# Kernel optimization log

Hardware: AMD Instinct MI355X
Metric: run time of the kernel (lower is better)

## Reference

```python
import jax, jax.numpy as jnp
import numpy as np

PRE_NMS_THRESH = 0.05
PRE_NMS_TOP_N = 1000
NMS_THRESH = 0.6
FPN_POST_NMS_TOP_N = 100
MIN_SIZE = 0
OFFSET = 10000.0  # per-class coordinate offset for batched per-class NMS
NEG = -1e9


def bilinear_resize(x, out_h, out_w):
    # x: [H, W, C] -> [out_h, out_w, C], matches torch interpolate(align_corners=False)
    H, W, _ = x.shape
    def grid(in_size, out_size):
        scale = in_size / out_size
        src = (jnp.arange(out_size, dtype=jnp.float32) + 0.5) * scale - 0.5
        src = jnp.clip(src, 0.0, in_size - 1.0)
        i0 = jnp.floor(src).astype(jnp.int32)
        i1 = jnp.minimum(i0 + 1, in_size - 1)
        lam = src - i0.astype(jnp.float32)
        return i0, i1, lam
    r0, r1, rl = grid(H, out_h)
    c0, c1, cl = grid(W, out_w)
    x = x[r0] * (1.0 - rl)[:, None, None] + x[r1] * rl[:, None, None]
    x = x[:, c0] * (1.0 - cl)[None, :, None] + x[:, c1] * cl[None, :, None]
    return x


def box_iou_plus1(b):
    area = (b[:, 2] - b[:, 0] + 1.0) * (b[:, 3] - b[:, 1] + 1.0)
    lt = jnp.maximum(b[:, None, :2], b[None, :, :2])
    rb = jnp.minimum(b[:, None, 2:], b[None, :, 2:])
    wh = jnp.clip(rb - lt + 1.0, 0.0)
    inter = wh[..., 0] * wh[..., 1]
    union = area[:, None] + area[None, :] - inter
    return inter / jnp.maximum(union, 1e-6)


def _forward(locations, box_cls, box_regression, centerness, box_mask, h, w):
    N, C, H, W = box_cls.shape
    M2 = box_mask.shape[1]
    Mi = int(np.sqrt(M2))
    HW = H * W
    K = PRE_NMS_TOP_N

    cls = jax.nn.sigmoid(box_cls.transpose(0, 2, 3, 1).reshape(N, HW, C))
    reg = box_regression.transpose(0, 2, 3, 1).reshape(N, HW, 4)
    cent = jax.nn.sigmoid(centerness.reshape(N, HW))
    mask = jax.nn.sigmoid(box_mask.transpose(0, 2, 3, 1))  # [N,H,W,M2]

    cand = cls > PRE_NMS_THRESH               # candidates from raw cls scores
    scr = cls * cent[:, :, None]              # centerness-weighted scores

    def per_image(cand_i, scr_i, reg_i, mask_i):
        # --- threshold + per-image topk (fixed K, padded with NEG) ---
        flat = jnp.where(cand_i, scr_i, NEG).reshape(HW * C)
        vals, idx = jax.lax.top_k(flat, K)
        valid = vals > NEG / 2
        loc_idx = idx // C
        labels = idx % C + 1                  # 1-based class labels
        locs = locations[loc_idx]             # [K,2]
        r = reg_i[loc_idx]                    # [K,4]
        boxes = jnp.stack([locs[:, 0] - r[:, 0], locs[:, 1] - r[:, 1],
                           locs[:, 0] + r[:, 2], locs[:, 1] + r[:, 3]], axis=1)
        scores = jnp.sqrt(jnp.where(valid, vals, 1.0)) * valid

        # --- mask paste: mean of upsampled mask over (buggy) box region ---
        up = bilinear_resize(mask_i, h, w)                      # [h,w,M2]
        integ = jnp.pad(jnp.cumsum(jnp.cumsum(up, 0), 1), ((1, 0), (1, 0), (0, 0)))
        bi = boxes.astype(jnp.int32)          # torch .int() truncation
        x1 = jnp.maximum(bi[:, 0], 0); x2 = jnp.minimum(bi[:, 2], h - 1)
        y1 = jnp.maximum(bi[:, 1], 0); y2 = jnp.minimum(bi[:, 3], w - 1)
        # original skip condition is (x1>=x2 or y1>=x2) -- bug replicated; extra
        # y1<y2 guard avoids NaN mean over empty region
        region_ok = (x1 < x2) & (y1 < x2) & (y1 < y2)
        x1c = jnp.clip(x1, 0, h); x2c = jnp.clip(x2, 0, h)
        y1c = jnp.clip(y1, 0, w); y2c = jnp.clip(y2, 0, w)
        s = integ[x2c, y2c] - integ[x1c, y2c] - integ[x2c, y1c] + integ[x1c, y1c]
        area = jnp.maximum((x2c - x1c) * (y2c - y1c), 1).astype(s.dtype)
        prob = ((s / area[:, None]) * region_ok[:, None]).reshape(K, Mi, Mi)

        # --- clip_to_image (x in [0,w-1], y in [0,h-1]) + remove_small_boxes ---
        bx = jnp.stack([jnp.clip(boxes[:, 0], 0, w - 1), jnp.clip(boxes[:, 1], 0, h - 1),
                        jnp.clip(boxes[:, 2], 0, w - 1), jnp.clip(boxes[:, 3], 0, h - 1)], 1)
        ws_ = bx[:, 2] - bx[:, 0] + 1.0
        hs_ = bx[:, 3] - bx[:, 1] + 1.0
        valid = valid & (ws_ >= MIN_SIZE) & (hs_ >= MIN_SIZE)

        # --- per-class greedy NMS via class-offset trick (fixed shape) ---
        nb = bx + (labels.astype(bx.dtype) * OFFSET)[:, None]
        order = jnp.argsort(-jnp.where(valid, scores, -1.0))
        nb_s, sc_s, v_s = nb[order], scores[order], valid[order]
        iou = box_iou_plus1(nb_s)
        rng = jnp.arange(K)
        def step(keep, i):
            ki = keep[i] & v_s[i]
            keep = keep.at[i].set(ki)
            keep = keep & ~(ki & (iou[i] > NMS_THRESH) & (rng > i))
            return keep, None
        keep, _ = jax.lax.scan(step, jnp.ones(K, bool), jnp.arange(K))
        v_final = keep & v_s

        # --- keep fpn_post_nms_top_n highest-scoring survivors ---
        fvals, fidx = jax.lax.top_k(jnp.where(v_final, sc_s, -1.0), FPN_POST_NMS_TOP_N)
        sel = order[fidx]
        vfin = v_final[fidx]
        return (bx[sel], scores[sel] * vfin, labels[sel], prob[sel] * vfin[:, None, None], vfin)

    return jax.vmap(per_image)(cand, scr, reg, mask)


def setup_inputs() -> dict:
    key = jax.random.key(0)
    ks = jax.random.split(key, 4)
    N, C, H, W, M2 = 2, 80, 32, 40, 196
    stride = 8
    ys, xs = jnp.meshgrid(jnp.arange(H), jnp.arange(W), indexing='ij')
    locations = jnp.stack([xs.reshape(-1), ys.reshape(-1)], 1).astype(jnp.float32) * stride + stride // 2
    box_cls = jax.random.normal(ks[0], (N, C, H, W), jnp.float32) - 2.0
    box_regression = jax.random.uniform(ks[1], (N, 4, H, W), jnp.float32) * 60.0 + 4.0
    centerness = jax.random.normal(ks[2], (N, 1, H, W), jnp.float32)
    box_mask = jax.random.normal(ks[3], (N, M2, H, W), jnp.float32)
    return {"locations": locations, "box_cls": box_cls, "box_regression": box_regression,
            "centerness": centerness, "box_mask": box_mask, "image_h": 256, "image_w": 320}


def reference(locations, box_cls, box_regression, centerness, box_mask, image_h, image_w):
    return _forward(locations, box_cls, box_regression, centerness, box_mask, image_h, image_w)
```

## Files before the change

kernel.cpp:

```cpp
#include <hip/hip_runtime.h>

#define DEVI __device__ __forceinline__

constexpr int N_ = 2, C_ = 80, H_ = 32, W_ = 40, HW_ = H_ * W_, HWC_ = HW_ * C_;
constexpr int KTOP = 1000, M2_ = 196;
constexpr int IMH = 256, IMW = 320;
constexpr int BUFCAP = 4096;
constexpr int NB = 2048;
constexpr int KB = 16;
constexpr int SLICE = HWC_ / KB;

constexpr int O_SC = 800, O_LB = 1000, O_PB = 1200, O_VF = 40400;

DEVI unsigned long long mapd(double v) {
  unsigned long long u = (unsigned long long)__double_as_longlong(v);
  return (u & 0x8000000000000000ull) ? ~u : (u | 0x8000000000000000ull);
}
DEVI double unmapd(unsigned long long k) {
  unsigned long long u = (k & 0x8000000000000000ull) ? (k ^ 0x8000000000000000ull) : ~k;
  return __longlong_as_double((long long)u);
}
DEVI int i0of(int x, int cap) {
  float src = ((float)x + 0.5f) * 0.125f - 0.5f;
  src = fminf(fmaxf(src, 0.f), (float)cap);
  return (int)floorf(src);
}

__global__ __launch_bounds__(1024) void k_pre(const float* cls, const float* cent, const float* bm,
                                              unsigned* ghist, unsigned* cand,
                                              float* msig, float* wr, float* wc) {
  int b = blockIdx.x, tid = threadIdx.x;
  if (b < N_ * KB) {
    __shared__ unsigned hist[NB];
    __shared__ unsigned run[NB];
    __shared__ unsigned short binls[SLICE];
    __shared__ float ce[HW_];
    __shared__ unsigned wtot[16], wabove[16];
    int n = b / KB, sb = b % KB;
    size_t base = (size_t)n * HWC_ + (size_t)sb * SLICE;
    for (int j = tid; j < NB; j += 1024) hist[j] = 0;
    for (int j = tid; j < HW_; j += 1024) ce[j] = 1.f / (1.f + expf(-cent[n * HW_ + j]));
    __syncthreads();
    #pragma unroll
    for (int it = 0; it < 7; ++it) {
      int j = it * 1024 + tid;
      if (j < SLICE) {
        float a = cls[base + j];
        float s = 1.f / (1.f + expf(-a));
        unsigned short bb = 0xFFFF;
        if (s > 0.0499999f) {
          float key = s * ce[j % HW_];
          unsigned kb2 = __float_as_uint(key);
          int bin = (int)(kb2 >> 16) - 0x3800;
          bin = bin < 0 ? 0 : (bin > NB - 1 ? NB - 1 : bin);
          bb = (unsigned short)bin;
          atomicAdd(&hist[bin], 1u);
        }
        binls[j] = bb;
      }
    }
    __syncthreads();
    unsigned* gh = ghist + ((size_t)n * KB + sb) * NB;
    for (int j = tid; j < NB; j += 1024) gh[j] = hist[j];
    int lane = tid & 63, wid = tid >> 6;
    unsigned aa = hist[2 * tid], bv = hist[2 * tid + 1];
    unsigned s2 = aa + bv, suf = s2;
    for (int off = 1; off < 64; off <<= 1) {
      unsigned v = __shfl_down(suf, off);
      if (lane + off < 64) suf += v;
    }
    if (lane == 0) wtot[wid] = suf;
    __syncthreads();
    if (tid == 0) { unsigned acc = 0; for (int w = 15; w >= 0; --w) { wabove[w] = acc; acc += wtot[w]; } }
    __syncthreads();
    unsigned above = (suf - s2) + wabove[wid];
    run[2 * tid + 1] = above;
    run[2 * tid] = above + bv;
    __syncthreads();
    unsigned* ca = cand + ((size_t)n * KB + sb) * SLICE;
    #pragma unroll
    for (int it = 0; it < 7; ++it) {
      int j = it * 1024 + tid;
      if (j < SLICE) {
        unsigned short bb = binls[j];
        if (bb != 0xFFFF) {
          unsigned pos = atomicAdd(&run[bb], 1u);
          ca[pos] = (unsigned)(base + j);
        }
      }
    }
  } else if (b < N_ * KB + 140) {
    __shared__ float tile[4][32][33];
    int g = tid >> 8, sub = tid & 255;
    int tt = (b - N_ * KB) * 4 + g;
    int n = tt / 280, r = tt % 280, rqt = r / 7, ct = r % 7;
    int tx = sub & 31, ty = sub >> 5;
    int rq0 = rqt * 32, c0 = ct * 32;
    for (int i = 0; i < 4; ++i) {
      int cc = c0 + ty + i * 8, rq = rq0 + tx;
      if (cc < M2_) {
        float v = bm[((size_t)n * M2_ + cc) * HW_ + rq];
        tile[g][ty + i * 8][tx] = 1.f / (1.f + expf(-v));
      }
    }
    __syncthreads();
    for (int i = 0; i < 4; ++i) {
      int rq = rq0 + ty + i * 8, cc = c0 + tx;
      if (cc < M2_) msig[((size_t)n * HW_ + rq) * M2_ + cc] = tile[g][tx][ty + i * 8];
    }
  } else {
    int t = tid;
    if (t < H_) {
      int r = t; float acc = 0.f; wr[0 * H_ + r] = 0.f;
      for (int x = 0; x < IMH; ++x) {
        float src = ((float)x + 0.5f) * ((float)H_ / (float)IMH) - 0.5f;
        src = fminf(fmaxf(src, 0.f), (float)(H_ - 1));
        int i0 = (int)floorf(src); int i1 = min(i0 + 1, H_ - 1);
        float lam = src - (float)i0;
        float w = ((r == i0) ? (1.f - lam) : 0.f) + ((r == i1) ? lam : 0.f);
        acc += w; wr[(x + 1) * H_ + r] = acc;
      }
    } else if (t < H_ + W_) {
      int q = t - H_; float acc = 0.f; wc[0 * W_ + q] = 0.f;
      for (int y = 0; y < IMW; ++y) {
        float src = ((float)y + 0.5f) * ((float)W_ / (float)IMW) - 0.5f;
        src = fminf(fmaxf(src, 0.f), (float)(W_ - 1));
        int i0 = (int)floorf(src); int i1 = min(i0 + 1, W_ - 1);
        float lam = src - (float)i0;
        float w = ((q == i0) ? (1.f - lam) : 0.f) + ((q == i1) ? lam : 0.f);
        acc += w; wc[(y + 1) * W_ + q] = acc;
      }
    }
  }
}

struct SortSh { unsigned long long K[BUFCAP]; unsigned I[BUFCAP]; };

__global__ __launch_bounds__(1024) void k_sel(const unsigned* ghist, const unsigned* cand,
                                              const float* cls, const float* cent,
                                              const float* loc, const float* breg,
                                              double* bxd, double* scd, int* lab, int* vld, int* rg,
                                              unsigned* keepg) {
  __shared__ SortSh sh;
  __shared__ unsigned wtot[16], wabove[16], sliceCnt[16], sliceOff[17];
  __shared__ unsigned sD;
  int n = blockIdx.x, tid = threadIdx.x, lane = tid & 63, wid = tid >> 6;
  keepg[n * 1024 + tid] = 0;
  const unsigned* gh = ghist + (size_t)n * KB * NB;
  unsigned a = 0, bv = 0;
  #pragma unroll
  for (int q = 0; q < KB; ++q) { a += gh[q * NB + 2 * tid]; bv += gh[q * NB + 2 * tid + 1]; }
  if (tid == 0) sD = 0;
  unsigned s2 = a + bv, suf = s2;
  for (int off = 1; off < 64; off <<= 1) {
    unsigned v = __shfl_down(suf, off);
    if (lane + off < 64) suf += v;
  }
  if (lane == 0) wtot[wid] = suf;
  __syncthreads();
  if (tid == 0) { unsigned acc = 0; for (int w = 15; w >= 0; --w) { wabove[w] = acc; acc += wtot[w]; } }
  __syncthreads();
  unsigned above = (suf - s2) + wabove[wid];
  if (above < 1000u && above + bv >= 1000u) sD = (unsigned)(2 * tid + 1);
  if (above + bv < 1000u && above + bv + a >= 1000u) sD = (unsigned)(2 * tid);
  __syncthreads();
  unsigned D = sD;
  unsigned Dg = (D > 0) ? D - 1 : 0;
  {
    unsigned acc = 0;
    for (int bin = (int)Dg + lane; bin < NB; bin += 64) acc += gh[wid * NB + bin];
    for (int off = 32; off; off >>= 1) acc += __shfl_down(acc, off);
    if (lane == 0) sliceCnt[wid] = acc;
  }
  __syncthreads();
  if (tid == 0) {
    unsigned acc = 0;
    for (int q = 0; q < KB; ++q) { sliceOff[q] = acc; acc += sliceCnt[q]; }
    sliceOff[KB] = acc;
  }
  __syncthreads();
  int G = (int)sliceOff[KB]; if (G > BUFCAP) G = BUFCAP;
  {
    const unsigned* ca = cand + ((size_t)n * KB + wid) * SLICE;
    unsigned cs = sliceCnt[wid], so = sliceOff[wid];
    for (unsigned e = lane; e < cs; e += 64) {
      unsigned pos = so + e;
      if (pos < (unsigned)BUFCAP) {
        unsigned t = ca[e];
        int c = (int)((t % (unsigned)HWC_) / (unsigned)HW_);
        int hw = (int)(t % (unsigned)HW_);
        double aa = (double)cls[t];
        double ss = 1.0 / (1.0 + exp(-aa));
        double ced = 1.0 / (1.0 + exp(-(double)cent[n * HW_ + hw]));
        double v = (ss > 0.05) ? ss * ced : -1e9;
        sh.K[pos] = mapd(v);
        sh.I[pos] = (unsigned)(hw * C_ + c);
      }
    }
  }
  __syncthreads();
  int P = 1024; while (P < G) P <<= 1;
  for (int j = G + tid; j < P; j += 1024) { sh.K[j] = 0ull; sh.I[j] = 0xFFFFFFFFu; }
  __syncthreads();
  int E = P >> 10;
  for (int sz = 2; sz <= P; sz <<= 1) {
    for (int st = sz >> 1; st >= 64; st >>= 1) {
      for (int p = tid; p < (P >> 1); p += 1024) {
        int i = ((p & ~(st - 1)) << 1) | (p & (st - 1));
        int j = i | st;
        bool up = ((i & sz) == 0);
        unsigned long long k1 = sh.K[i], k2 = sh.K[j];
        unsigned i1 = sh.I[i], i2 = sh.I[j];
        bool bef = (k1 > k2) || (k1 == k2 && i1 < i2);
        if (bef != up) { sh.K[i] = k2; sh.K[j] = k1; sh.I[i] = i2; sh.I[j] = i1; }
      }
      __syncthreads();
    }
    {
      int st0 = ((sz >> 1) < 32) ? (sz >> 1) : 32;
      for (int e = 0; e < E; ++e) {
        int elem = tid + (e << 10);
        unsigned long long k = sh.K[elem];
        unsigned ii = sh.I[elem];
        bool dir = ((elem & sz) == 0);
        for (int st = st0; st >= 1; st >>= 1) {
          unsigned long long ko = __shfl_xor(k, st);
          unsigned io = __shfl_xor(ii, st);
          bool low = ((elem & st) == 0);
          bool first = (k > ko) || (k == ko && ii < io);
          bool take_mine = first ^ (!low) ^ (!dir);
          if (!take_mine) { k = ko; ii = io; }
        }
        sh.K[elem] = k; sh.I[elem] = ii;
      }
      __syncthreads();
    }
  }

  if (tid < KTOP) {
    unsigned long long key = sh.K[tid];
    unsigned idx = sh.I[tid];
    double v = unmapd(key);
    int valid = (v > -5e8) && (idx < (unsigned)HWC_);
    if (idx >= (unsigned)HWC_) idx = 0;
    int hw = (int)(idx / C_), c = (int)(idx % C_);
    double lx = (double)loc[hw * 2 + 0], ly = (double)loc[hw * 2 + 1];
    const float* rg4 = breg + (size_t)n * 4 * HW_;
    double r0 = (double)rg4[0 * HW_ + hw], r1 = (double)rg4[1 * HW_ + hw];
    double r2 = (double)rg4[2 * HW_ + hw], r3 = (double)rg4[3 * HW_ + hw];
    double b0 = lx - r0, b1 = ly - r1, b2 = lx + r2, b3 = ly + r3;
    double sc = valid ? sqrt(v) : 0.0;
    int bi0 = (int)b0, bi1 = (int)b1, bi2 = (int)b2, bi3 = (int)b3;
    int x1 = max(bi0, 0), x2 = min(bi2, IMH - 1), y1 = max(bi1, 0), y2 = min(bi3, IMW - 1);
    int rok = (x1 < x2) && (y1 < x2) && (y1 < y2);
    int x1c = min(max(x1, 0), IMH), x2c = min(max(x2, 0), IMH);
    int y1c = min(max(y1, 0), IMW), y2c = min(max(y2, 0), IMW);
    int area = max((x2c - x1c) * (y2c - y1c), 1);
    double c0 = fmin(fmax(b0, 0.0), (double)(IMW - 1));
    double c1 = fmin(fmax(b1, 0.0), (double)(IMH - 1));
    double c2 = fmin(fmax(b2, 0.0), (double)(IMW - 1));
    double c3 = fmin(fmax(b3, 0.0), (double)(IMH - 1));
    size_t base = (size_t)n * 1024 + tid;
    bxd[base * 4 + 0] = c0; bxd[base * 4 + 1] = c1; bxd[base * 4 + 2] = c2; bxd[base * 4 + 3] = c3;
    scd[base] = sc; lab[base] = c + 1; vld[base] = valid;
    int* r8 = rg + base * 8;
    r8[0] = x1c; r8[1] = x2c; r8[2] = y1c; r8[3] = y2c; r8[4] = area; r8[5] = rok;
  }
}

__global__ void k_nms(const double* bxd, const int* lab, const int* vld, unsigned* keepg) {
  int cls = blockIdx.x + 1, n = blockIdx.y, tid = threadIdx.x;
  __shared__ int mk[KTOP];
  __shared__ double mb0[KTOP], mb1[KTOP], mb2[KTOP], mb3[KTOP], ma[KTOP];
  __shared__ unsigned char kept[KTOP];
  int m = 0;
  for (int base = 0; base < KTOP; base += 64) {
    int t = base + tid;
    bool pred = (t < KTOP) && (lab[n * 1024 + t] == cls) && (vld[n * 1024 + t] != 0);
    unsigned long long bb = __ballot(pred);
    if (pred) {
      int pos = m + (int)__popcll(bb & ((1ull << tid) - 1ull));
      mk[pos] = t;
      const double* p = bxd + ((size_t)n * 1024 + t) * 4;
      double b0 = p[0], b1 = p[1], b2 = p[2], b3 = p[3];
      mb0[pos] = b0; mb1[pos] = b1; mb2[pos] = b2; mb3[pos] = b3;
      ma[pos] = (b2 - b0 + 1.0) * (b3 - b1 + 1.0);
      kept[pos] = 1;
    }
    m += (int)__popcll(bb);
  }
  __syncthreads();
  for (int i = 0; i < m; ++i) {
    if (kept[i]) {
      double x1 = mb0[i], y1 = mb1[i], x2 = mb2[i], y2 = mb3[i], ai = ma[i];
      for (int j = i + 1 + tid; j < m; j += 64) {
        double ltx = fmax(x1, mb0[j]), lty = fmax(y1, mb1[j]);
        double rbx = fmin(x2, mb2[j]), rby = fmin(y2, mb3[j]);
        double iw = fmax(rbx - ltx + 1.0, 0.0), ih = fmax(rby - lty + 1.0, 0.0);
        double inter = iw * ih;
        double uni = ai + ma[j] - inter;
        if (inter / fmax(uni, 1e-6) > 0.6) kept[j] = 0;
      }
    }
    __syncthreads();
  }
  for (int i = tid; i < m; i += 64) keepg[n * 1024 + mk[i]] = (unsigned)kept[i];
}

__global__ __launch_bounds__(256) void k_finish(const unsigned* keepg, const double* bxd,
                                                const double* scd, const int* lab, const int* rg,
                                                const float* msig, const float* wr, const float* wc,
                                                float* out) {
  int t = blockIdx.x, n = blockIdx.y, tid = threadIdx.x, lane = tid & 63, wid = tid >> 6;
  __shared__ int lsel[100], lvf[100];
  __shared__ unsigned woff[4]; __shared__ unsigned sS;
  __shared__ float A[H_], B[W_];

  int i0 = tid * 4;
  unsigned ff[4]; int lc = 0;
  for (int j = 0; j < 4; ++j) {
    int i = i0 + j;
    ff[j] = (i < KTOP) ? keepg[n * 1024 + i] : 0u;
    lc += (int)ff[j];
  }
  unsigned pre = (unsigned)lc;
  for (int off = 1; off < 64; off <<= 1) {
    unsigned v = __shfl_up(pre, off);
    if (lane >= off) pre += v;
  }
  if (lane == 63) woff[wid] = pre;
  __syncthreads();
  if (tid == 0) { unsigned acc = 0; for (int w = 0; w < 4; ++w) { unsigned tmp = woff[w]; woff[w] = acc; acc += tmp; } sS = acc; }
  __syncthreads();
  int kpre = (int)(woff[wid] + pre - (unsigned)lc);
  int S = (int)sS;
  for (int j = 0; j < 4; ++j) {
    int i = i0 + j;
    if (i < KTOP) {
      if (ff[j]) { if (kpre < 100) { lsel[kpre] = i; lvf[kpre] = 1; } kpre++; }
      else { int slot = S + (i - kpre); if (slot < 100) { lsel[slot] = i; lvf[slot] = 0; } }
    }
  }
  __syncthreads();

  int k = lsel[t], vf = lvf[t];
  if (tid == 0) {
    const double* bb = bxd + ((size_t)n * 1024 + k) * 4;
    out[(n * 100 + t) * 4 + 0] = (float)bb[0];
    out[(n * 100 + t) * 4 + 1] = (float)bb[1];
    out[(n * 100 + t) * 4 + 2] = (float)bb[2];
    out[(n * 100 + t) * 4 + 3] = (float)bb[3];
    out[O_SC + n * 100 + t] = vf ? (float)scd[n * 1024 + k] : 0.f;
    out[O_LB + n * 100 + t] = (float)lab[n * 1024 + k];
    out[O_VF + n * 100 + t] = (float)vf;
  }
  const int* r8 = rg + ((size_t)n * 1024 + k) * 8;
  int x1c = r8[0], x2c = r8[1], y1c = r8[2], y2c = r8[3], area = r8[4], rok = r8[5];
  if (tid < H_) A[tid] = wr[x2c * H_ + tid] - wr[x1c * H_ + tid];
  else if (tid < H_ + W_) { int q = tid - H_; B[q] = wc[y2c * W_ + q] - wc[y1c * W_ + q]; }
  __syncthreads();
  if (tid < M2_) {
    float acc = 0.f;
    if (rok && vf) {
      int rlo = i0of(x1c, H_ - 1);
      int rhi = min(i0of(x2c - 1, H_ - 1) + 1, H_ - 1);
      int qlo = i0of(y1c, W_ - 1);
      int qhi = min(i0of(y2c - 1, W_ - 1) + 1, W_ - 1);
      for (int r = rlo; r <= rhi; ++r) {
        float ar = A[r];
        const float* mrow = msig + ((size_t)((n * H_ + r) * W_ + qlo)) * M2_ + tid;
        float rs = 0.f;
        #pragma unroll 4
        for (int q = qlo; q <= qhi; ++q) { rs += B[q] * mrow[0]; mrow += M2_; }
        acc += ar * rs;
      }
      acc /= (float)area;
    }
    out[O_PB + (size_t)(n * 100 + t) * M2_ + tid] = acc;
  }
}

extern "C" void kernel_launch(void* const* d_in, const int* in_sizes, int n_in,
                              void* d_out, int out_size, void* d_ws, size_t ws_size,
                              hipStream_t stream) {
  (void)in_sizes; (void)n_in; (void)out_size; (void)ws_size;
  const float* locations = (const float*)d_in[0];
  const float* box_cls   = (const float*)d_in[1];
  const float* box_reg   = (const float*)d_in[2];
  const float* cent      = (const float*)d_in[3];
  const float* box_mask  = (const float*)d_in[4];
  float* out = (float*)d_out;

  char* ws = (char*)d_ws;
  size_t off = 0;
  auto alloc = [&](size_t bytes) -> void* {
    void* p = ws + off;
    off = (off + bytes + 255) & ~(size_t)255;
    return p;
  };
  unsigned* ghist = (unsigned*)alloc((size_t)N_ * KB * NB * 4);
  unsigned* cand  = (unsigned*)alloc((size_t)N_ * KB * SLICE * 4);
  double* bxd     = (double*)alloc((size_t)N_ * 1024 * 4 * 8);
  double* scd     = (double*)alloc((size_t)N_ * 1024 * 8);
  int* lab        = (int*)alloc((size_t)N_ * 1024 * 4);
  int* vld        = (int*)alloc((size_t)N_ * 1024 * 4);
  int* rg         = (int*)alloc((size_t)N_ * 1024 * 8 * 4);
  unsigned* keepg = (unsigned*)alloc((size_t)N_ * 1024 * 4);
  float* msig     = (float*)alloc((size_t)N_ * HW_ * M2_ * 4);
  float* wr       = (float*)alloc((size_t)(IMH + 1) * H_ * 4);
  float* wc       = (float*)alloc((size_t)(IMW + 1) * W_ * 4);

  k_pre<<<N_ * KB + 140 + 1, 1024, 0, stream>>>(box_cls, cent, box_mask, ghist, cand, msig, wr, wc);
  k_sel<<<N_, 1024, 0, stream>>>(ghist, cand, box_cls, cent, locations, box_reg,
                                 bxd, scd, lab, vld, rg, keepg);
  k_nms<<<dim3(C_, N_), 64, 0, stream>>>(bxd, lab, vld, keepg);
  k_finish<<<dim3(100, N_), 256, 0, stream>>>(keepg, bxd, scd, lab, rg, msig, wr, wc, out);
}
```

Baseline: 100.9 us.

## Fuse four-stage pipeline into one cooperative kernel with grid syncs

Merges the preprocessing, top-k selection, per-class NMS and mask-finish kernels into a single cooperative kernel of 200 blocks separated by grid-wide syncs. Candidate compaction now happens inside the histogram blocks, using the global threshold bin and wave-ballot offsets, writing at most 2048 candidates per image. This replaces the separate full-slice candidate lists. NMS uses one wave per class with ballot-based suppression bitmasks and caps each class at 128 boxes. The aim is to remove launch gaps and shrink the gather and sort, at the cost of grid-sync overhead, 1024-thread blocks that sit idle in most phases, and a cap that could change results if a class has more than 128 boxes.

Result: slower. 179.2 us (+77.7%).

```diff
diff --git a/kernel.cpp b/kernel.cpp
--- a/kernel.cpp
+++ b/kernel.cpp
@@ -1,14 +1,18 @@
 #include <hip/hip_runtime.h>
+#include <hip/hip_cooperative_groups.h>
+
+namespace cg = cooperative_groups;
 
 #define DEVI __device__ __forceinline__
 
 constexpr int N_ = 2, C_ = 80, H_ = 32, W_ = 40, HW_ = H_ * W_, HWC_ = HW_ * C_;
 constexpr int KTOP = 1000, M2_ = 196;
 constexpr int IMH = 256, IMW = 320;
-constexpr int BUFCAP = 4096;
 constexpr int NB = 2048;
 constexpr int KB = 16;
 constexpr int SLICE = HWC_ / KB;
+constexpr int BCAP = 2048;
+constexpr int GBLK = 200;
 
 constexpr int O_SC = 800, O_LB = 1000, O_PB = 1200, O_VF = 40400;
 
@@ -26,71 +30,55 @@
   return (int)floorf(src);
 }
 
-__global__ __launch_bounds__(1024) void k_pre(const float* cls, const float* cent, const float* bm,
-                                              unsigned* ghist, unsigned* cand,
-                                              float* msig, float* wr, float* wc) {
-  int b = blockIdx.x, tid = threadIdx.x;
+struct ShSlice {
+  unsigned key[SLICE];
+  unsigned hist[NB];
+  float ce[HW_];
+  unsigned wtot[16], wabove[16], sliceCnt[16], sliceOff[17];
+  unsigned sD, lcnt;
+};
+struct ShSort { unsigned long long K[BCAP]; unsigned I[BCAP]; };
+struct ShNms  { double bx[128][5]; unsigned short ml[128]; };
+struct ShMask { float tile[4][32][33]; };
+struct ShFin  { int lsel[100], lvf[100]; unsigned wcnt[16], woff[16], Stot; float A[H_], Bw[W_]; };
+union ShU { ShSlice a; ShSort c; ShNms d; ShMask m; ShFin e; };
+
+__global__ __launch_bounds__(1024) void mega(const float* cls, const float* cent, const float* bm,
+                                             const float* loc, const float* breg,
+                                             unsigned* ghist, unsigned* bufI, unsigned* cntG,
+                                             double* bxd, double* scd, int* lab, int* vld, int* rg,
+                                             unsigned* keepg, float* msig, float* wr, float* wc,
+                                             float* out) {
+  __shared__ ShU sh;
+  cg::grid_group gg = cg::this_grid();
+  int b = blockIdx.x, tid = threadIdx.x, lane = tid & 63, wid = tid >> 6;
+
   if (b < N_ * KB) {
-    __shared__ unsigned hist[NB];
-    __shared__ unsigned run[NB];
-    __shared__ unsigned short binls[SLICE];
-    __shared__ float ce[HW_];
-    __shared__ unsigned wtot[16], wabove[16];
-    int n = b / KB, sb = b % KB;
+    int n = b >> 4, sb = b & 15;
     size_t base = (size_t)n * HWC_ + (size_t)sb * SLICE;
-    for (int j = tid; j < NB; j += 1024) hist[j] = 0;
-    for (int j = tid; j < HW_; j += 1024) ce[j] = 1.f / (1.f + expf(-cent[n * HW_ + j]));
+    for (int j = tid; j < NB; j += 1024) sh.a.hist[j] = 0;
+    for (int j = tid; j < HW_; j += 1024) sh.a.ce[j] = 1.f / (1.f + expf(-cent[n * HW_ + j]));
     __syncthreads();
     #pragma unroll
     for (int it = 0; it < 7; ++it) {
       int j = it * 1024 + tid;
       if (j < SLICE) {
-        float a = cls[base + j];
-        float s = 1.f / (1.f + expf(-a));
-        unsigned short bb = 0xFFFF;
+        float aa = cls[base + j];
+        float s = 1.f / (1.f + expf(-aa));
+        unsigned key = 0;
         if (s > 0.0499999f) {
-          float key = s * ce[j % HW_];
-          unsigned kb2 = __float_as_uint(key);
-          int bin = (int)(kb2 >> 16) - 0x3800;
+          key = __float_as_uint(s * sh.a.ce[j % HW_]);
+          int bin = (int)(key >> 16) - 0x3800;
           bin = bin < 0 ? 0 : (bin > NB - 1 ? NB - 1 : bin);
-          bb = (unsigned short)bin;
-          atomicAdd(&hist[bin], 1u);
-        }
-        binls[j] = bb;
+          atomicAdd(&sh.a.hist[bin], 1u);
+        }
+        sh.a.key[j] = key;
       }
     }
     __syncthreads();
     unsigned* gh = ghist + ((size_t)n * KB + sb) * NB;
-    for (int j = tid; j < NB; j += 1024) gh[j] = hist[j];
-    int lane = tid & 63, wid = tid >> 6;
-    unsigned aa = hist[2 * tid], bv = hist[2 * tid + 1];
-    unsigned s2 = aa + bv, suf = s2;
-    for (int off = 1; off < 64; off <<= 1) {
-      unsigned v = __shfl_down(suf, off);
-      if (lane + off < 64) suf += v;
-    }
-    if (lane == 0) wtot[wid] = suf;
-    __syncthreads();
-    if (tid == 0) { unsigned acc = 0; for (int w = 15; w >= 0; --w) { wabove[w] = acc; acc += wtot[w]; } }
-    __syncthreads();
-    unsigned above = (suf - s2) + wabove[wid];
-    run[2 * tid + 1] = above;
-    run[2 * tid] = above + bv;
-    __syncthreads();
-    unsigned* ca = cand + ((size_t)n * KB + sb) * SLICE;
-    #pragma unroll
-    for (int it = 0; it < 7; ++it) {
-      int j = it * 1024 + tid;
-      if (j < SLICE) {
-        unsigned short bb = binls[j];
-        if (bb != 0xFFFF) {
-          unsigned pos = atomicAdd(&run[bb], 1u);
-          ca[pos] = (unsigned)(base + j);
-        }
-      }
-    }
+    for (int j = tid; j < NB; j += 1024) gh[j] = sh.a.hist[j];
   } else if (b < N_ * KB + 140) {
-    __shared__ float tile[4][32][33];
     int g = tid >> 8, sub = tid & 255;
     int tt = (b - N_ * KB) * 4 + g;
     int n = tt / 280, r = tt % 280, rqt = r / 7, ct = r % 7;
@@ -100,15 +88,15 @@
       int cc = c0 + ty + i * 8, rq = rq0 + tx;
       if (cc < M2_) {
         float v = bm[((size_t)n * M2_ + cc) * HW_ + rq];
-        tile[g][ty + i * 8][tx] = 1.f / (1.f + expf(-v));
+        sh.m.tile[g][ty + i * 8][tx] = 1.f / (1.f + expf(-v));
       }
     }
     __syncthreads();
     for (int i = 0; i < 4; ++i) {
       int rq = rq0 + ty + i * 8, cc = c0 + tx;
-      if (cc < M2_) msig[((size_t)n * HW_ + rq) * M2_ + cc] = tile[g][tx][ty + i * 8];
-    }
-  } else {
+      if (cc < M2_) msig[((size_t)n * HW_ + rq) * M2_ + cc] = sh.m.tile[g][tx][ty + i * 8];
+    }
+  } else if (b == N_ * KB + 140) {
     int t = tid;
     if (t < H_) {
       int r = t; float acc = 0.f; wr[0 * H_ + r] = 0.f;
@@ -132,251 +120,267 @@
       }
     }
   }
-}
-
-struct SortSh { unsigned long long K[BUFCAP]; unsigned I[BUFCAP]; };
-
-__global__ __launch_bounds__(1024) void k_sel(const unsigned* ghist, const unsigned* cand,
-                                              const float* cls, const float* cent,
-                                              const float* loc, const float* breg,
-                                              double* bxd, double* scd, int* lab, int* vld, int* rg,
-                                              unsigned* keepg) {
-  __shared__ SortSh sh;
-  __shared__ unsigned wtot[16], wabove[16], sliceCnt[16], sliceOff[17];
-  __shared__ unsigned sD;
-  int n = blockIdx.x, tid = threadIdx.x, lane = tid & 63, wid = tid >> 6;
-  keepg[n * 1024 + tid] = 0;
-  const unsigned* gh = ghist + (size_t)n * KB * NB;
-  unsigned a = 0, bv = 0;
-  #pragma unroll
-  for (int q = 0; q < KB; ++q) { a += gh[q * NB + 2 * tid]; bv += gh[q * NB + 2 * tid + 1]; }
-  if (tid == 0) sD = 0;
-  unsigned s2 = a + bv, suf = s2;
-  for (int off = 1; off < 64; off <<= 1) {
-    unsigned v = __shfl_down(suf, off);
-    if (lane + off < 64) suf += v;
+  gg.sync();
+
+  if (b < N_ * KB) {
+    int n = b >> 4, sb = b & 15;
+    const unsigned* gh = ghist + (size_t)n * KB * NB;
+    unsigned a = 0, bv = 0;
+    #pragma unroll
+    for (int q = 0; q < KB; ++q) { a += gh[q * NB + 2 * tid]; bv += gh[q * NB + 2 * tid + 1]; }
+    if (tid == 0) { sh.a.sD = 0; sh.a.lcnt = 0; }
+    unsigned s2 = a + bv, suf = s2;
+    for (int off = 1; off < 64; off <<= 1) {
+      unsigned v = __shfl_down(suf, off);
+      if (lane + off < 64) suf += v;
+    }
+    if (lane == 0) sh.a.wtot[wid] = suf;
+    __syncthreads();
+    if (tid == 0) { unsigned acc = 0; for (int w = 15; w >= 0; --w) { sh.a.wabove[w] = acc; acc += sh.a.wtot[w]; } }
+    __syncthreads();
+    unsigned above = (suf - s2) + sh.a.wabove[wid];
+    if (above < 1000u && above + bv >= 1000u) sh.a.sD = (unsigned)(2 * tid + 1);
+    if (above + bv < 1000u && above + bv + a >= 1000u) sh.a.sD = (unsigned)(2 * tid);
+    __syncthreads();
+    unsigned D = sh.a.sD;
+    unsigned Dg = (D > 0) ? D - 1 : 0;
+    {
+      unsigned acc = 0;
+      for (int bin = (int)Dg + lane; bin < NB; bin += 64) acc += gh[wid * NB + bin];
+      for (int off = 32; off; off >>= 1) acc += __shfl_down(acc, off);
+      if (lane == 0) sh.a.sliceCnt[wid] = acc;
+    }
+    __syncthreads();
+    if (tid == 0) {
+      unsigned acc = 0;
+      for (int q = 0; q < KB; ++q) { sh.a.sliceOff[q] = acc; acc += sh.a.sliceCnt[q]; }
+      sh.a.sliceOff[KB] = acc;
+      if (sb == 0) cntG[n] = acc;
+    }
+    __syncthreads();
+    unsigned myStart = sh.a.sliceOff[sb];
+    #pragma unroll
+    for (int it = 0; it < 7; ++it) {
+      int j = it * 1024 + tid;
+      bool win = false;
+      if (j < SLICE) {
+        unsigned key = sh.a.key[j];
+        if (key) {
+          int bin = (int)(key >> 16) - 0x3800;
+          bin = bin < 0 ? 0 : (bin > NB - 1 ? NB - 1 : bin);
+          win = (unsigned)bin >= Dg;
+        }
+      }
+      unsigned long long mb = __ballot(win);
+      if (mb) {
+        int lead = __builtin_ctzll(mb);
+        unsigned offw = 0;
+        if (lane == lead) offw = atomicAdd(&sh.a.lcnt, (unsigned)__popcll(mb));
+        offw = (unsigned)__shfl((int)offw, lead);
+        if (win) {
+          unsigned pos = myStart + offw + (unsigned)__popcll(mb & ((1ull << lane) - 1ull));
+          if (pos < (unsigned)BCAP)
+            bufI[(size_t)n * BCAP + pos] = (unsigned)((j % HW_) * C_ + (sb * 5 + j / HW_));
+        }
+      }
+    }
   }
-  if (lane == 0) wtot[wid] = suf;
-  __syncthreads();
-  if (tid == 0) { unsigned acc = 0; for (int w = 15; w >= 0; --w) { wabove[w] = acc; acc += wtot[w]; } }
-  __syncthreads();
-  unsigned above = (suf - s2) + wabove[wid];
-  if (above < 1000u && above + bv >= 1000u) sD = (unsigned)(2 * tid + 1);
-  if (above + bv < 1000u && above + bv + a >= 1000u) sD = (unsigned)(2 * tid);
-  __syncthreads();
-  unsigned D = sD;
-  unsigned Dg = (D > 0) ? D - 1 : 0;
+  gg.sync();
+
+  if (b < N_) {
+    int n = b;
+    unsigned cnt = cntG[n]; if (cnt > (unsigned)BCAP) cnt = BCAP;
+    for (unsigned pos = tid; pos < cnt; pos += 1024) {
+      unsigned idx = bufI[(size_t)n * BCAP + pos];
+      int hw = (int)(idx / C_), c = (int)(idx % C_);
+      double aa = (double)cls[(size_t)n * HWC_ + (size_t)c * HW_ + hw];
+      double ss = 1.0 / (1.0 + exp(-aa));
+      double ced = 1.0 / (1.0 + exp(-(double)cent[n * HW_ + hw]));
+      double v = (ss > 0.05) ? ss * ced : -1e9;
+      sh.c.K[pos] = mapd(v);
+      sh.c.I[pos] = idx;
+    }
+    int P = 1024; while (P < (int)cnt) P <<= 1;
+    for (int j = (int)cnt + tid; j < P; j += 1024) { sh.c.K[j] = 0ull; sh.c.I[j] = 0xFFFFFFFFu; }
+    __syncthreads();
+    int E = P >> 10;
+    for (int sz = 2; sz <= P; sz <<= 1) {
+      for (int st = sz >> 1; st >= 64; st >>= 1) {
+        for (int p = tid; p < (P >> 1); p += 1024) {
+          int i = ((p & ~(st - 1)) << 1) | (p & (st - 1));
+          int j = i | st;
+          bool up = ((i & sz) == 0);
+          unsigned long long k1 = sh.c.K[i], k2 = sh.c.K[j];
+          unsigned i1 = sh.c.I[i], i2 = sh.c.I[j];
+          bool bef = (k1 > k2) || (k1 == k2 && i1 < i2);
+          if (bef != up) { sh.c.K[i] = k2; sh.c.K[j] = k1; sh.c.I[i] = i2; sh.c.I[j] = i1; }
+        }
+        __syncthreads();
+      }
+      {
+        int st0 = ((sz >> 1) < 32) ? (sz >> 1) : 32;
+        for (int e = 0; e < E; ++e) {
+          int elem = tid + (e << 10);
+          unsigned long long k = sh.c.K[elem];
+          unsigned ii = sh.c.I[elem];
+          bool dir = ((elem & sz) == 0);
+          for (int st = st0; st >= 1; st >>= 1) {
+            unsigned long long ko = __shfl_xor(k, st);
+            unsigned io = __shfl_xor(ii, st);
+            bool low = ((elem & st) == 0);
+            bool first = (k > ko) || (k == ko && ii < io);
+            bool take_mine = first ^ (!low) ^ (!dir);
+            if (!take_mine) { k = ko; ii = io; }
+          }
+          sh.c.K[elem] = k; sh.c.I[elem] = ii;
+        }
+        __syncthreads();
+      }
+    }
+    if (tid < KTOP) {
+      unsigned long long key = sh.c.K[tid];
+      unsigned idx = sh.c.I[tid];
+      double v = unmapd(key);
+      int valid = (v > -5e8) && (idx < (unsigned)HWC_);
+      if (idx >= (unsigned)HWC_) idx = 0;
+      int hw = (int)(idx / C_), c = (int)(idx % C_);
+      double lx = (double)loc[hw * 2 + 0], ly = (double)loc[hw * 2 + 1];
+      const float* rg4 = breg + (size_t)n * 4 * HW_;
+      double r0 = (double)rg4[0 * HW_ + hw], r1 = (double)rg4[1 * HW_ + hw];
+      double r2 = (double)rg4[2 * HW_ + hw], r3 = (double)rg4[3 * HW_ + hw];
+      double b0 = lx - r0, b1 = ly - r1, b2 = lx + r2, b3 = ly + r3;
+      double sc = valid ? sqrt(v) : 0.0;
+      int bi0 = (int)b0, bi1 = (int)b1, bi2 = (int)b2, bi3 = (int)b3;
+      int x1 = max(bi0, 0), x2 = min(bi2, IMH - 1), y1 = max(bi1, 0), y2 = min(bi3, IMW - 1);
+      int rok = (x1 < x2) && (y1 < x2) && (y1 < y2);
+      int x1c = min(max(x1, 0), IMH), x2c = min(max(x2, 0), IMH);
+      int y1c = min(max(y1, 0), IMW), y2c = min(max(y2, 0), IMW);
+      int area = max((x2c - x1c) * (y2c - y1c), 1);
+      double c0 = fmin(fmax(b0, 0.0), (double)(IMW - 1));
+      double c1 = fmin(fmax(b1, 0.0), (double)(IMH - 1));
+      double c2 = fmin(fmax(b2, 0.0), (double)(IMW - 1));
+      double c3 = fmin(fmax(b3, 0.0), (double)(IMH - 1));
+      size_t base = (size_t)n * 1024 + tid;
+      bxd[base * 4 + 0] = c0; bxd[base * 4 + 1] = c1; bxd[base * 4 + 2] = c2; bxd[base * 4 + 3] = c3;
+      scd[base] = sc; lab[base] = c + 1; vld[base] = valid;
+      int* r8 = rg + base * 8;
+      r8[0] = x1c; r8[1] = x2c; r8[2] = y1c; r8[3] = y2c; r8[4] = area; r8[5] = rok;
+    }
+  } else if (b < N_ + 2) {
+    keepg[(b - N_) * 1024 + tid] = 0;
+  }
+  gg.sync();
+
+  if (b < N_ * C_) {
+    int cls_ = (b % C_) + 1, n = b / C_;
+    if (tid < 64) {
+      int m = 0;
+      for (int ch = 0; ch < 16; ++ch) {
+        int e = ch * 64 + lane;
+        bool pred = (e < KTOP) && vld[n * 1024 + e] && (lab[n * 1024 + e] == cls_);
+        unsigned long long bb = __ballot(pred);
+        if (pred) {
+          int pos = m + (int)__popcll(bb & ((1ull << lane) - 1ull));
+          if (pos < 128) {
+            const double* p = bxd + ((size_t)n * 1024 + e) * 4;
+            double b0 = p[0], b1 = p[1], b2 = p[2], b3 = p[3];
+            sh.d.bx[pos][0] = b0; sh.d.bx[pos][1] = b1; sh.d.bx[pos][2] = b2; sh.d.bx[pos][3] = b3;
+            sh.d.bx[pos][4] = (b2 - b0 + 1.0) * (b3 - b1 + 1.0);
+            sh.d.ml[pos] = (unsigned short)e;
+          }
+        }
+        m += (int)__popcll(bb);
+      }
+      if (m > 128) m = 128;
+      __builtin_amdgcn_wave_barrier();
+      unsigned long long k0 = (m >= 64) ? ~0ull : ((1ull << m) - 1ull);
+      unsigned long long k1m = (m > 64) ? ((m >= 128) ? ~0ull : ((1ull << (m - 64)) - 1ull)) : 0ull;
+      for (int i = 0; i < m; ++i) {
+        bool alive = (i < 64) ? ((k0 >> i) & 1ull) : ((k1m >> (i - 64)) & 1ull);
+        if (!alive) continue;
+        double x1 = sh.d.bx[i][0], y1 = sh.d.bx[i][1], x2 = sh.d.bx[i][2], y2 = sh.d.bx[i][3], ai = sh.d.bx[i][4];
+        {
+          int j = lane;
+          bool ok = (j < m) && (j > i);
+          int jj = ok ? j : 0;
+          double u1 = sh.d.bx[jj][0], v1 = sh.d.bx[jj][1], u2 = sh.d.bx[jj][2], v2 = sh.d.bx[jj][3], aj = sh.d.bx[jj][4];
+          double ltx = fmax(x1, u1), lty = fmax(y1, v1), rbx = fmin(x2, u2), rby = fmin(y2, v2);
+          double iw = fmax(rbx - ltx + 1.0, 0.0), ih = fmax(rby - lty + 1.0, 0.0);
+          double inter = iw * ih, uni = ai + aj - inter;
+          bool sup = ok && (inter / fmax(uni, 1e-6) > 0.6);
+          k0 &= ~__ballot(sup);
+        }
+        if (m > 64) {
+          int j = 64 + lane;
+          bool ok = (j < m) && (j > i);
+          int jj = ok ? j : 0;
+          double u1 = sh.d.bx[jj][0], v1 = sh.d.bx[jj][1], u2 = sh.d.bx[jj][2], v2 = sh.d.bx[jj][3], aj = sh.d.bx[jj][4];
+          double ltx = fmax(x1, u1), lty = fmax(y1, v1), rbx = fmin(x2, u2), rby = fmin(y2, v2);
+          double iw = fmax(rbx - ltx + 1.0, 0.0), ih = fmax(rby - lty + 1.0, 0.0);
+          double inter = iw * ih, uni = ai + aj - inter;
+          bool sup = ok && (inter / fmax(uni, 1e-6) > 0.6);
+          k1m &= ~__ballot(sup);
+        }
+      }
+      for (int j = lane; j < m; j += 64) {
+        bool kb = (j < 64) ? ((k0 >> j) & 1ull) : ((k1m >> (j - 64)) & 1ull);
+        keepg[n * 1024 + sh.d.ml[j]] = kb ? 1u : 0u;
+      }
+    }
+  }
+  gg.sync();
+
   {
-    unsigned acc = 0;
-    for (int bin = (int)Dg + lane; bin < NB; bin += 64) acc += gh[wid * NB + bin];
-    for (int off = 32; off; off >>= 1) acc += __shfl_down(acc, off);
-    if (lane == 0) sliceCnt[wid] = acc;
-  }
-  __syncthreads();
-  if (tid == 0) {
-    unsigned acc = 0;
-    for (int q = 0; q < KB; ++q) { sliceOff[q] = acc; acc += sliceCnt[q]; }
-    sliceOff[KB] = acc;
-  }
-  __syncthreads();
-  int G = (int)sliceOff[KB]; if (G > BUFCAP) G = BUFCAP;
-  {
-    const unsigned* ca = cand + ((size_t)n * KB + wid) * SLICE;
-    unsigned cs = sliceCnt[wid], so = sliceOff[wid];
-    for (unsigned e = lane; e < cs; e += 64) {
-      unsigned pos = so + e;
-      if (pos < (unsigned)BUFCAP) {
-        unsigned t = ca[e];
-        int c = (int)((t % (unsigned)HWC_) / (unsigned)HW_);
-        int hw = (int)(t % (unsigned)HW_);
-        double aa = (double)cls[t];
-        double ss = 1.0 / (1.0 + exp(-aa));
-        double ced = 1.0 / (1.0 + exp(-(double)cent[n * HW_ + hw]));
-        double v = (ss > 0.05) ? ss * ced : -1e9;
-        sh.K[pos] = mapd(v);
-        sh.I[pos] = (unsigned)(hw * C_ + c);
-      }
-    }
-  }
-  __syncthreads();
-  int P = 1024; while (P < G) P <<= 1;
-  for (int j = G + tid; j < P; j += 1024) { sh.K[j] = 0ull; sh.I[j] = 0xFFFFFFFFu; }
-  __syncthreads();
-  int E = P >> 10;
-  for (int sz = 2; sz <= P; sz <<= 1) {
-    for (int st = sz >> 1; st >= 64; st >>= 1) {
-      for (int p = tid; p < (P >> 1); p += 1024) {
-        int i = ((p & ~(st - 1)) << 1) | (p & (st - 1));
-        int j = i | st;
-        bool up = ((i & sz) == 0);
-        unsigned long long k1 = sh.K[i], k2 = sh.K[j];
-        unsigned i1 = sh.I[i], i2 = sh.I[j];
-        bool bef = (k1 > k2) || (k1 == k2 && i1 < i2);
-        if (bef != up) { sh.K[i] = k2; sh.K[j] = k1; sh.I[i] = i2; sh.I[j] = i1; }
-      }
-      __syncthreads();
-    }
-    {
-      int st0 = ((sz >> 1) < 32) ? (sz >> 1) : 32;
-      for (int e = 0; e < E; ++e) {
-        int elem = tid + (e << 10);
-        unsigned long long k = sh.K[elem];
-        unsigned ii = sh.I[elem];
-        bool dir = ((elem & sz) == 0);
-        for (int st = st0; st >= 1; st >>= 1) {
-          unsigned long long ko = __shfl_xor(k, st);
-          unsigned io = __shfl_xor(ii, st);
-          bool low = ((elem & st) == 0);
-          bool first = (k > ko) || (k == ko && ii < io);
-          bool take_mine = first ^ (!low) ^ (!dir);
-          if (!take_mine) { k = ko; ii = io; }
-        }
-        sh.K[elem] = k; sh.I[elem] = ii;
-      }
-      __syncthreads();
-    }
-  }
-
-  if (tid < KTOP) {
-    unsigned long long key = sh.K[tid];
-    unsigned idx = sh.I[tid];
-    double v = unmapd(key);
-    int valid = (v > -5e8) && (idx < (unsigned)HWC_);
-    if (idx >= (unsigned)HWC_) idx = 0;
-    int hw = (int)(idx / C_), c = (int)(idx % C_);
-    double lx = (double)loc[hw * 2 + 0], ly = (double)loc[hw * 2 + 1];
-    const float* rg4 = breg + (size_t)n * 4 * HW_;
-    double r0 = (double)rg4[0 * HW_ + hw], r1 = (double)rg4[1 * HW_ + hw];
-    double r2 = (double)rg4[2 * HW_ + hw], r3 = (double)rg4[3 * HW_ + hw];
-    double b0 = lx - r0, b1 = ly - r1, b2 = lx + r2, b3 = ly + r3;
-    double sc = valid ? sqrt(v) : 0.0;
-    int bi0 = (int)b0, bi1 = (int)b1, bi2 = (int)b2, bi3 = (int)b3;
-    int x1 = max(bi0, 0), x2 = min(bi2, IMH - 1), y1 = max(bi1, 0), y2 = min(bi3, IMW - 1);
-    int rok = (x1 < x2) && (y1 < x2) && (y1 < y2);
-    int x1c = min(max(x1, 0), IMH), x2c = min(max(x2, 0), IMH);
-    int y1c = min(max(y1, 0), IMW), y2c = min(max(y2, 0), IMW);
-    int area = max((x2c - x1c) * (y2c - y1c), 1);
-    double c0 = fmin(fmax(b0, 0.0), (double)(IMW - 1));
-    double c1 = fmin(fmax(b1, 0.0), (double)(IMH - 1));
-    double c2 = fmin(fmax(b2, 0.0), (double)(IMW - 1));
-    double c3 = fmin(fmax(b3, 0.0), (double)(IMH - 1));
-    size_t base = (size_t)n * 1024 + tid;
-    bxd[base * 4 + 0] = c0; bxd[base * 4 + 1] = c1; bxd[base * 4 + 2] = c2; bxd[base * 4 + 3] = c3;
-    scd[base] = sc; lab[base] = c + 1; vld[base] = valid;
-    int* r8 = rg + base * 8;
-    r8[0] = x1c; r8[1] = x2c; r8[2] = y1c; r8[3] = y2c; r8[4] = area; r8[5] = rok;
-  }
-}
-
-__global__ void k_nms(const double* bxd, const int* lab, const int* vld, unsigned* keepg) {
-  int cls = blockIdx.x + 1, n = blockIdx.y, tid = threadIdx.x;
-  __shared__ int mk[KTOP];
-  __shared__ double mb0[KTOP], mb1[KTOP], mb2[KTOP], mb3[KTOP], ma[KTOP];
-  __shared__ unsigned char kept[KTOP];
-  int m = 0;
-  for (int base = 0; base < KTOP; base += 64) {
-    int t = base + tid;
-    bool pred = (t < KTOP) && (lab[n * 1024 + t] == cls) && (vld[n * 1024 + t] != 0);
-    unsigned long long bb = __ballot(pred);
-    if (pred) {
-      int pos = m + (int)__popcll(bb & ((1ull << tid) - 1ull));
-      mk[pos] = t;
-      const double* p = bxd + ((size_t)n * 1024 + t) * 4;
-      double b0 = p[0], b1 = p[1], b2 = p[2], b3 = p[3];
-      mb0[pos] = b0; mb1[pos] = b1; mb2[pos] = b2; mb3[pos] = b3;
-      ma[pos] = (b2 - b0 + 1.0) * (b3 - b1 + 1.0);
-      kept[pos] = 1;
-    }
-    m += (int)__popcll(bb);
-  }
-  __syncthreads();
-  for (int i = 0; i < m; ++i) {
-    if (kept[i]) {
-      double x1 = mb0[i], y1 = mb1[i], x2 = mb2[i], y2 = mb3[i], ai = ma[i];
-      for (int j = i + 1 + tid; j < m; j += 64) {
-        double ltx = fmax(x1, mb0[j]), lty = fmax(y1, mb1[j]);
-        double rbx = fmin(x2, mb2[j]), rby = fmin(y2, mb3[j]);
-        double iw = fmax(rbx - ltx + 1.0, 0.0), ih = fmax(rby - lty + 1.0, 0.0);
-        double inter = iw * ih;
-        double uni = ai + ma[j] - inter;
-        if (inter / fmax(uni, 1e-6) > 0.6) kept[j] = 0;
-      }
-    }
-    __syncthreads();
-  }
-  for (int i = tid; i < m; i += 64) keepg[n * 1024 + mk[i]] = (unsigned)kept[i];
-}
-
-__global__ __launch_bounds__(256) void k_finish(const unsigned* keepg, const double* bxd,
-                                                const double* scd, const int* lab, const int* rg,
-                                                const float* msig, const float* wr, const float* wc,
-                                                float* out) {
-  int t = blockIdx.x, n = blockIdx.y, tid = threadIdx.x, lane = tid & 63, wid = tid >> 6;
-  __shared__ int lsel[100], lvf[100];
-  __shared__ unsigned woff[4]; __shared__ unsigned sS;
-  __shared__ float A[H_], B[W_];
-
-  int i0 = tid * 4;
-  unsigned ff[4]; int lc = 0;
-  for (int j = 0; j < 4; ++j) {
-    int i = i0 + j;
-    ff[j] = (i < KTOP) ? keepg[n * 1024 + i] : 0u;
-    lc += (int)ff[j];
-  }
-  unsigned pre = (unsigned)lc;
-  for (int off = 1; off < 64; off <<= 1) {
-    unsigned v = __shfl_up(pre, off);
-    if (lane >= off) pre += v;
-  }
-  if (lane == 63) woff[wid] = pre;
-  __syncthreads();
-  if (tid == 0) { unsigned acc = 0; for (int w = 0; w < 4; ++w) { unsigned tmp = woff[w]; woff[w] = acc; acc += tmp; } sS = acc; }
-  __syncthreads();
-  int kpre = (int)(woff[wid] + pre - (unsigned)lc);
-  int S = (int)sS;
-  for (int j = 0; j < 4; ++j) {
-    int i = i0 + j;
-    if (i < KTOP) {
-      if (ff[j]) { if (kpre < 100) { lsel[kpre] = i; lvf[kpre] = 1; } kpre++; }
-      else { int slot = S + (i - kpre); if (slot < 100) { lsel[slot] = i; lvf[slot] = 0; } }
-    }
-  }
-  __syncthreads();
-
-  int k = lsel[t], vf = lvf[t];
-  if (tid == 0) {
-    const double* bb = bxd + ((size_t)n * 1024 + k) * 4;
-    out[(n * 100 + t) * 4 + 0] = (float)bb[0];
-    out[(n * 100 + t) * 4 + 1] = (float)bb[1];
-    out[(n * 100 + t) * 4 + 2] = (float)bb[2];
-    out[(n * 100 + t) * 4 + 3] = (float)bb[3];
-    out[O_SC + n * 100 + t] = vf ? (float)scd[n * 1024 + k] : 0.f;
-    out[O_LB + n * 100 + t] = (float)lab[n * 1024 + k];
-    out[O_VF + n * 100 + t] = (float)vf;
-  }
-  const int* r8 = rg + ((size_t)n * 1024 + k) * 8;
-  int x1c = r8[0], x2c = r8[1], y1c = r8[2], y2c = r8[3], area = r8[4], rok = r8[5];
-  if (tid < H_) A[tid] = wr[x2c * H_ + tid] - wr[x1c * H_ + tid];
-  else if (tid < H_ + W_) { int q = tid - H_; B[q] = wc[y2c * W_ + q] - wc[y1c * W_ + q]; }
-  __syncthreads();
-  if (tid < M2_) {
-    float acc = 0.f;
-    if (rok && vf) {
-      int rlo = i0of(x1c, H_ - 1);
-      int rhi = min(i0of(x2c - 1, H_ - 1) + 1, H_ - 1);
-      int qlo = i0of(y1c, W_ - 1);
-      int qhi = min(i0of(y2c - 1, W_ - 1) + 1, W_ - 1);
-      for (int r = rlo; r <= rhi; ++r) {
-        float ar = A[r];
-        const float* mrow = msig + ((size_t)((n * H_ + r) * W_ + qlo)) * M2_ + tid;
-        float rs = 0.f;
-        #pragma unroll 4
-        for (int q = qlo; q <= qhi; ++q) { rs += B[q] * mrow[0]; mrow += M2_; }
-        acc += ar * rs;
-      }
-      acc /= (float)area;
-    }
-    out[O_PB + (size_t)(n * 100 + t) * M2_ + tid] = acc;
+    int t = b % 100, n = b / 100;
+    int kp = (tid < KTOP) ? (int)keepg[n * 1024 + tid] : 0;
+    unsigned long long bal = __ballot(kp != 0);
+    int posw = (int)__popcll(bal & ((1ull << lane) - 1ull));
+    if (lane == 0) sh.e.wcnt[wid] = (unsigned)__popcll(bal);
+    __syncthreads();
+    if (tid == 0) { unsigned acc = 0; for (int i = 0; i < 16; ++i) { sh.e.woff[i] = acc; acc += sh.e.wcnt[i]; } sh.e.Stot = acc; }
+    __syncthreads();
+    int posK = (int)sh.e.woff[wid] + posw;
+    int S = (int)sh.e.Stot;
+    if (tid < KTOP) {
+      if (kp) { if (posK < 100) { sh.e.lsel[posK] = tid; sh.e.lvf[posK] = 1; } }
+      else { int slot = S + (tid - posK); if (slot < 100) { sh.e.lsel[slot] = tid; sh.e.lvf[slot] = 0; } }
+    }
+    __syncthreads();
+    int k = sh.e.lsel[t], vf = sh.e.lvf[t];
+    if (tid == 0) {
+      const double* bb = bxd + ((size_t)n * 1024 + k) * 4;
+      out[(n * 100 + t) * 4 + 0] = (float)bb[0];
+      out[(n * 100 + t) * 4 + 1] = (float)bb[1];
+      out[(n * 100 + t) * 4 + 2] = (float)bb[2];
+      out[(n * 100 + t) * 4 + 3] = (float)bb[3];
+      out[O_SC + n * 100 + t] = vf ? (float)scd[n * 1024 + k] : 0.f;
+      out[O_LB + n * 100 + t] = (float)lab[n * 1024 + k];
+      out[O_VF + n * 100 + t] = (float)vf;
+    }
+    const int* r8 = rg + ((size_t)n * 1024 + k) * 8;
+    int x1c = r8[0], x2c = r8[1], y1c = r8[2], y2c = r8[3], area = r8[4], rok = r8[5];
+    if (tid < H_) sh.e.A[tid] = wr[x2c * H_ + tid] - wr[x1c * H_ + tid];
+    else if (tid < H_ + W_) { int q = tid - H_; sh.e.Bw[q] = wc[y2c * W_ + q] - wc[y1c * W_ + q]; }
+    __syncthreads();
+    if (tid < M2_) {
+      float acc = 0.f;
+      if (rok && vf) {
+        int rlo = i0of(x1c, H_ - 1);
+        int rhi = min(i0of(x2c - 1, H_ - 1) + 1, H_ - 1);
+        int qlo = i0of(y1c, W_ - 1);
+        int qhi = min(i0of(y2c - 1, W_ - 1) + 1, W_ - 1);
+        for (int r = rlo; r <= rhi; ++r) {
+          float ar = sh.e.A[r];
+          const float* mrow = msig + ((size_t)((n * H_ + r) * W_ + qlo)) * M2_ + tid;
+          float rs = 0.f;
+          #pragma unroll 4
+          for (int q = qlo; q <= qhi; ++q) { rs += sh.e.Bw[q] * mrow[0]; mrow += M2_; }
+          acc += ar * rs;
+        }
+        acc /= (float)area;
+      }
+      out[O_PB + (size_t)(n * 100 + t) * M2_ + tid] = acc;
+    }
   }
 }
 
@@ -399,7 +403,8 @@
     return p;
   };
   unsigned* ghist = (unsigned*)alloc((size_t)N_ * KB * NB * 4);
-  unsigned* cand  = (unsigned*)alloc((size_t)N_ * KB * SLICE * 4);
+  unsigned* bufI  = (unsigned*)alloc((size_t)N_ * BCAP * 4);
+  unsigned* cntG  = (unsigned*)alloc(16 * 4);
   double* bxd     = (double*)alloc((size_t)N_ * 1024 * 4 * 8);
   double* scd     = (double*)alloc((size_t)N_ * 1024 * 8);
   int* lab        = (int*)alloc((size_t)N_ * 1024 * 4);
@@ -410,9 +415,9 @@
   float* wr       = (float*)alloc((size_t)(IMH + 1) * H_ * 4);
   float* wc       = (float*)alloc((size_t)(IMW + 1) * W_ * 4);
 
-  k_pre<<<N_ * KB + 140 + 1, 1024, 0, stream>>>(box_cls, cent, box_mask, ghist, cand, msig, wr, wc);
-  k_sel<<<N_, 1024, 0, stream>>>(ghist, cand, box_cls, cent, locations, box_reg,
-                                 bxd, scd, lab, vld, rg, keepg);
-  k_nms<<<dim3(C_, N_), 64, 0, stream>>>(bxd, lab, vld, keepg);
-  k_finish<<<dim3(100, N_), 256, 0, stream>>>(keepg, bxd, scd, lab, rg, msig, wr, wc, out);
+  void* args[] = { (void*)&box_cls, (void*)&cent, (void*)&box_mask, (void*)&locations, (void*)&box_reg,
+                   (void*)&ghist, (void*)&bufI, (void*)&cntG, (void*)&bxd, (void*)&scd,
+                   (void*)&lab, (void*)&vld, (void*)&rg, (void*)&keepg, (void*)&msig,
+                   (void*)&wr, (void*)&wc, (void*)&out };
+  hipLaunchCooperativeKernel((void*)mega, dim3(GBLK), dim3(1024), args, 0, stream);
 }
```
